# Optimization experiments

Measured on AMD Instinct MI355X. Metric: run time of the kernel, lower is better.

## Reference

```python
import jax, jax.numpy as jnp
import numpy as np

B, T, E, H, FF = 8, 1024, 1024, 16, 4096
HD = E // H
SCALE = HD ** -0.5
EPS = 1e-12  # LayerNorm eps from TransformerLayer


def layer_norm(x, w, b):
    u = x.mean(-1, keepdims=True)
    s = ((x - u) ** 2).mean(-1, keepdims=True)  # biased variance, as in module
    return w * (x - u) / jnp.sqrt(s + EPS) + b


def setup_inputs() -> dict:
    key = jax.random.key(0)
    ks = jax.random.split(key, 8)
    std = 0.02  # nn.init.normal_(std=0.02)
    x = jax.random.normal(ks[0], (B, T, E), jnp.float32)
    # padding mask: positions >= length are padding (1 = ignore); ensure no all-masked row
    lengths = jax.random.randint(ks[1], (B,), T // 2, T + 1)
    self_padding_mask = jnp.arange(T)[None, :] >= lengths[:, None]
    # causal mask from SelfAttentionMask: triu(ones, 1)
    attn_mask = jnp.triu(jnp.ones((T, T), dtype=bool), 1)
    in_w = std * jax.random.normal(ks[2], (3 * E, E), jnp.float32)
    in_b = jnp.zeros((3 * E,), jnp.float32)
    out_w = std * jax.random.normal(ks[3], (E, E), jnp.float32)
    out_b = jnp.zeros((E,), jnp.float32)
    fc1_w = std * jax.random.normal(ks[4], (FF, E), jnp.float32)
    fc1_b = jnp.zeros((FF,), jnp.float32)
    fc2_w = std * jax.random.normal(ks[5], (E, FF), jnp.float32)
    fc2_b = jnp.zeros((E,), jnp.float32)
    ln1_w = jnp.ones((E,), jnp.float32)
    ln1_b = jnp.zeros((E,), jnp.float32)
    ln2_w = jnp.ones((E,), jnp.float32)
    ln2_b = jnp.zeros((E,), jnp.float32)
    return dict(x=x, in_w=in_w, in_b=in_b, out_w=out_w, out_b=out_b,
                fc1_w=fc1_w, fc1_b=fc1_b, fc2_w=fc2_w, fc2_b=fc2_b,
                ln1_w=ln1_w, ln1_b=ln1_b, ln2_w=ln2_w, ln2_b=ln2_b,
                self_padding_mask=self_padding_mask, attn_mask=attn_mask)


def reference(x, in_w, in_b, out_w, out_b, fc1_w, fc1_b, fc2_w, fc2_b,
              ln1_w, ln1_b, ln2_w, ln2_b, self_padding_mask, attn_mask):
    b, t, e = x.shape
    # --- self attention sublayer ---
    residual = x
    qkv = x @ in_w.T + in_b                       # [B,T,3E] fused in_proj (qkv_same path)
    q, k, v = jnp.split(qkv, 3, axis=-1)
    q = (q * SCALE).reshape(b, t, H, HD)
    k = k.reshape(b, t, H, HD)
    v = v.reshape(b, t, H, HD)
    scores = jnp.einsum('bqhd,bkhd->bhqk', q, k)  # [B,H,T,T]
    mask = attn_mask[None, None, :, :] | self_padding_mask[:, None, None, :]
    scores = jnp.where(mask, -jnp.inf, scores)
    p = jax.nn.softmax(scores, axis=-1)
    attn = jnp.einsum('bhqk,bkhd->bqhd', p, v).reshape(b, t, e)
    attn = attn @ out_w.T + out_b
    x = layer_norm(residual + attn, ln1_w, ln1_b)
    # --- feed-forward sublayer ---
    residual = x
    h = jax.nn.relu(x @ fc1_w.T + fc1_b)
    x = layer_norm(residual + (h @ fc2_w.T + fc2_b), ln2_w, ln2_b)
    return x
```

## Files before the change

kernel.cpp:

```cpp
#include <hip/hip_runtime.h>

typedef unsigned short u16;
typedef __attribute__((ext_vector_type(8))) short short8;
typedef __attribute__((ext_vector_type(4))) short short4v;
typedef __attribute__((ext_vector_type(4))) float f32x4;

#define DEV static __device__ __forceinline__

DEV float bf2f(u16 h) {
    union { unsigned int u; float f; } v; v.u = ((unsigned int)h) << 16; return v.f;
}
DEV u16 f2bf(float f) {
    union { float f; unsigned int u; } v; v.f = f;
    unsigned int r = (v.u + 0x7fff + ((v.u >> 16) & 1)) >> 16;
    return (u16)r;
}
DEV float ldx(const void* p, size_t i, int f32) {
    return f32 ? ((const float*)p)[i] : bf2f(((const u16*)p)[i]);
}

#define GLD16(g, l) __builtin_amdgcn_global_load_lds( \
    (const __attribute__((address_space(1))) void*)(g), \
    (__attribute__((address_space(3))) void*)(l), 16, 0, 0)

#define STAGE(P, pf32, eoff, dst8) do {                                        \
    if (!(pf32)) { GLD16(((const u16*)(P)) + (eoff), (dst8)); }                \
    else {                                                                     \
        const float* _p = ((const float*)(P)) + (eoff);                        \
        f32x4 _a = *(const f32x4*)_p, _b = *(const f32x4*)(_p + 4);            \
        short8 _s;                                                             \
        _s[0]=(short)f2bf(_a[0]); _s[1]=(short)f2bf(_a[1]);                    \
        _s[2]=(short)f2bf(_a[2]); _s[3]=(short)f2bf(_a[3]);                    \
        _s[4]=(short)f2bf(_b[0]); _s[5]=(short)f2bf(_b[1]);                    \
        _s[6]=(short)f2bf(_b[2]); _s[7]=(short)f2bf(_b[3]);                    \
        *(short8*)(dst8) = _s;                                                 \
    } } while (0)

__global__ __launch_bounds__(64) void probe_kernel(
    const void* __restrict__ x, const void* __restrict__ pad,
    int* __restrict__ flags, int* __restrict__ flagsA)
{
    const int lane = threadIdx.x;
    const u16* xu = (const u16*)x;
    const unsigned int e = (xu[lane * 2] >> 7) & 0xFF;
    const int sane = (e >= 0x70 && e <= 0x8F) ? 1 : 0;
    unsigned long long m = __ballot(sane);
    const int f32 = (__popcll(m) < 32) ? 1 : 0;

    const unsigned int* pi = (const unsigned int*)pad;
    int bytes = 0;
#pragma unroll
    for (int j = 0; j < 6; j++) {
        unsigned int v = pi[128 + j * 64 + lane];
        if (v > 1u) bytes = 1;
    }
    m = __ballot(bytes);
    if (lane == 0) {
        flags[0] = f32; flags[1] = (m != 0ULL) ? 1 : 0;
        flagsA[0] = 0;  flagsA[1] = 0;
    }
}

__global__ __launch_bounds__(256) void conv4(
    const void* __restrict__ src, u16* __restrict__ dst, int n4,
    const int* __restrict__ flags)
{
    const int i = blockIdx.x * 256 + threadIdx.x;
    if (i >= n4) return;
    if (flags[0]) {
        f32x4 v = ((const f32x4*)src)[i];
        short4v s;
        s[0] = (short)f2bf(v[0]); s[1] = (short)f2bf(v[1]);
        s[2] = (short)f2bf(v[2]); s[3] = (short)f2bf(v[3]);
        ((short4v*)dst)[i] = s;
    } else {
        ((short4v*)dst)[i] = ((const short4v*)src)[i];
    }
}

__global__ __launch_bounds__(256) void mask_to_bias(
    const void* __restrict__ pad, float* __restrict__ out,
    const int* __restrict__ flags)
{
    const int i = blockIdx.x * 256 + threadIdx.x;
    const int mv = flags[1] ? (int)((const unsigned char*)pad)[i]
                            : ((const int*)pad)[i];
    out[i] = mv ? -1e30f : 0.0f;
}

#define GEMM_CORE(Av, ASEL, a_row0, Wv, w_off, ldw, K)                        \
    __shared__ __align__(16) u16 As[128 * 32];                                \
    __shared__ __align__(16) u16 Bs[128 * 32];                                \
    const int inf32 = flags[0];                                               \
    const int af32  = (ASEL) ? inf32 : 0;                                     \
    const int tid  = threadIdx.x;                                             \
    const int lane = tid & 63;                                                \
    const int wave = tid >> 6;                                                \
    const int lc   = lane & 15;                                               \
    const int quad = lane >> 4;                                               \
    const int m0 = blockIdx.x * 128;                                          \
    const int n0 = blockIdx.y * 128;                                          \
    const int wm = (wave >> 1) * 64;                                          \
    const int wn = (wave & 1) * 64;                                           \
    const int r0 = tid >> 2;                                                  \
    const int ko = (tid & 3) * 8;                                             \
    f32x4 acc[4][4] = {};                                                     \
    for (int k0 = 0; k0 < (K); k0 += 32) {                                    \
        STAGE(Av, af32, ((size_t)(a_row0) + m0 + r0) * (K) + k0 + ko,         \
              &As[tid * 8]);                                                  \
        STAGE(Av, af32, ((size_t)(a_row0) + m0 + r0 + 64) * (K) + k0 + ko,    \
              &As[2048 + tid * 8]);                                           \
        STAGE(Wv, inf32, (size_t)(w_off) + (size_t)(n0 + r0) * (ldw) + k0 + ko,\
              &Bs[tid * 8]);                                                  \
        STAGE(Wv, inf32, (size_t)(w_off) + (size_t)(n0 + r0 + 64) * (ldw) + k0 + ko,\
              &Bs[2048 + tid * 8]);                                           \
        __syncthreads();                                                      \
        short8 afr[4], bfr[4];                                                \
        const int qd = quad * 8;                                              \
        _Pragma("unroll")                                                     \
        for (int mt = 0; mt < 4; mt++)                                        \
            afr[mt] = *(const short8*)&As[(wm + mt * 16 + lc) * 32 + qd];     \
        _Pragma("unroll")                                                     \
        for (int nt = 0; nt < 4; nt++)                                        \
            bfr[nt] = *(const short8*)&Bs[(wn + nt * 16 + lc) * 32 + qd];     \
        _Pragma("unroll")                                                     \
        for (int mt = 0; mt < 4; mt++)                                        \
            _Pragma("unroll")                                                 \
            for (int nt = 0; nt < 4; nt++)                                    \
                acc[mt][nt] = __builtin_amdgcn_mfma_f32_16x16x32_bf16(        \
                    afr[mt], bfr[nt], acc[mt][nt], 0, 0, 0);                  \
        __syncthreads();                                                      \
    }                                                                         \
    const int ce0 = n0 + wn + lc;                                             \
    const int re0 = m0 + wm + quad * 4;

template<int EPI>
__global__ __launch_bounds__(256, 2) void gemm_bt(
    const void* __restrict__ A, int a_sel, long a_row0,
    const void* __restrict__ W, long w_off,
    const void* __restrict__ bias, long b_off,
    const void* __restrict__ resid, int r_sel, long r_row0,
    u16* __restrict__ C, long c_row0,
    int N, int K, int ldw, const int* __restrict__ flags)
{
    GEMM_CORE(A, a_sel, a_row0, W, w_off, ldw, K)
    const int rf32 = r_sel ? inf32 : 0;
#pragma unroll
    for (int mt = 0; mt < 4; mt++) {
#pragma unroll
        for (int nt = 0; nt < 4; nt++) {
            const int c = ce0 + nt * 16;
            const float bv = ldx(bias, (size_t)b_off + c, inf32);
#pragma unroll
            for (int i = 0; i < 4; i++) {
                const int r = re0 + mt * 16 + i;
                float v = acc[mt][nt][i] + bv;
                if (EPI == 1)
                    v += ldx(resid, ((size_t)r_row0 + r) * N + c, rf32);
                if (EPI == 2) v = fmaxf(v, 0.0f);
                C[((size_t)c_row0 + r) * N + c] = f2bf(v);
            }
        }
    }
}

__global__ __launch_bounds__(256, 2) void gemm_qkv(
    const void* __restrict__ A, long a_row0,
    const void* __restrict__ W, const void* __restrict__ bias,
    u16* __restrict__ Qo, u16* __restrict__ Ko, u16* __restrict__ Vt,
    const int* __restrict__ flags)
{
    GEMM_CORE(A, 1, a_row0, W, 0, 1024, 1024)
    if (n0 < 1024) {
#pragma unroll
        for (int mt = 0; mt < 4; mt++)
#pragma unroll
            for (int nt = 0; nt < 4; nt++) {
                const int c = ce0 + nt * 16;
                const float bv = ldx(bias, c, inf32);
#pragma unroll
                for (int i = 0; i < 4; i++) {
                    const int r = re0 + mt * 16 + i;
                    Qo[((size_t)a_row0 + r) * 1024 + c] =
                        f2bf((acc[mt][nt][i] + bv) * 0.125f);
                }
            }
    } else if (n0 < 2048) {
#pragma unroll
        for (int mt = 0; mt < 4; mt++)
#pragma unroll
            for (int nt = 0; nt < 4; nt++) {
                const int c = ce0 + nt * 16;
                const float bv = ldx(bias, c, inf32);
#pragma unroll
                for (int i = 0; i < 4; i++) {
                    const int r = re0 + mt * 16 + i;
                    Ko[(size_t)r * 1024 + (c - 1024)] = f2bf(acc[mt][nt][i] + bv);
                }
            }
    } else {
#pragma unroll
        for (int mt = 0; mt < 4; mt++)
#pragma unroll
            for (int nt = 0; nt < 4; nt++) {
                const int c = ce0 + nt * 16;
                const float bv = ldx(bias, c, inf32);
                const int cv = c - 2048;
                const int hh = cv >> 6, d = cv & 63;
                const int rb = re0 + mt * 16;
                const int bl = rb >> 10, t = rb & 1023;
                short4v pk;
#pragma unroll
                for (int i = 0; i < 4; i++)
                    pk[i] = (short)f2bf(acc[mt][nt][i] + bv);
                *(short4v*)&Vt[((size_t)(bl * 16 + hh) * 64 + d) * 1024 + t] = pk;
            }
    }
}

__global__ __launch_bounds__(256, 2) void gemm_accf32(
    const void* __restrict__ A, const void* __restrict__ W, long w_off,
    const void* __restrict__ bias, const u16* __restrict__ resid, long r_row0,
    float* __restrict__ C, int ldw, int init, const int* __restrict__ flags)
{
    GEMM_CORE(A, 0, 0, W, w_off, ldw, 1024)
#pragma unroll
    for (int mt = 0; mt < 4; mt++) {
#pragma unroll
        for (int nt = 0; nt < 4; nt++) {
            const int c = ce0 + nt * 16;
            const float bv = ldx(bias, c, inf32);
#pragma unroll
            for (int i = 0; i < 4; i++) {
                const int r = re0 + mt * 16 + i;
                float v = acc[mt][nt][i];
                if (init) v += bv + bf2f(resid[((size_t)r_row0 + r) * 1024 + c]);
                else      v += C[(size_t)r * 1024 + c];
                C[(size_t)r * 1024 + c] = v;
            }
        }
    }
}

#define GEMM8_PRE(Ag_, Wg_, Kg_)                                              \
    __shared__ __align__(16) u16 Ab[3][128 * 64];                             \
    __shared__ __align__(16) u16 Bb[3][256 * 64];                             \
    const u16* Ag = (Ag_); const u16* Wg = (Wg_); const int Kg = (Kg_);       \
    const int tid  = threadIdx.x;                                             \
    const int lane = tid & 63;                                                \
    const int lc   = lane & 15;                                               \
    const int quad = lane >> 4;                                               \
    const int w    = tid >> 6;                                                \
    const int wr   = w >> 2;                                                  \
    const int wc   = w & 3;                                                   \
    const int m0 = blockIdx.x * 128;                                          \
    const int n0 = blockIdx.y * 256;                                          \
    const int srow = tid >> 3;                                                \
    const int scol = (((tid & 7) ^ (srow & 7)) << 3);                         \
    const int sw0 = (((quad) ^ (lc & 7)) << 3);                               \
    const int sw1 = sw0 ^ 32;                                                 \
    f32x4 acc[4][4] = {};                                                     \
    short8 af[4], bf[4];

#define SA8(buf, kk) do {                                                     \
    GLD16(Ag + (size_t)(m0 + srow) * Kg + (kk) + scol, &Ab[buf][tid * 8]);    \
    GLD16(Ag + (size_t)(m0 + 64 + srow) * Kg + (kk) + scol,                   \
          &Ab[buf][4096 + tid * 8]); } while (0)
#define SB8a(buf, kk) do {                                                    \
    GLD16(Wg + (size_t)(n0 + srow) * Kg + (kk) + scol, &Bb[buf][tid * 8]);    \
    GLD16(Wg + (size_t)(n0 + 64 + srow) * Kg + (kk) + scol,                   \
          &Bb[buf][4096 + tid * 8]); } while (0)
#define SB8b(buf, kk) do {                                                    \
    GLD16(Wg + (size_t)(n0 + 128 + srow) * Kg + (kk) + scol,                  \
          &Bb[buf][8192 + tid * 8]);                                          \
    GLD16(Wg + (size_t)(n0 + 192 + srow) * Kg + (kk) + scol,                  \
          &Bb[buf][12288 + tid * 8]); } while (0)
#define LDFR(rbuf, SW) do { _Pragma("unroll")                                 \
    for (int q_ = 0; q_ < 4; q_++) {                                          \
        af[q_] = *(const short8*)&Ab[rbuf][(wr * 64 + q_ * 16 + lc) * 64 + (SW)];\
        bf[q_] = *(const short8*)&Bb[rbuf][(wc * 64 + q_ * 16 + lc) * 64 + (SW)];\
    } } while (0)
#define MFMA16 do { _Pragma("unroll")                                         \
    for (int mq = 0; mq < 4; mq++) { _Pragma("unroll")                        \
    for (int nq = 0; nq < 4; nq++)                                            \
        acc[mq][nq] = __builtin_amdgcn_mfma_f32_16x16x32_bf16(                \
            af[mq], bf[nq], acc[mq][nq], 0, 0, 0); } } while (0)

#define GEMM8_LOOP                                                            \
    const int NT = Kg >> 6;                                                   \
    SA8(0, 0); SB8a(0, 0); SB8b(0, 0);                                        \
    if (NT > 1) { SA8(1, 64); SB8a(1, 64); SB8b(1, 64); }                     \
    if (NT > 1) asm volatile("s_waitcnt vmcnt(6)" ::: "memory");              \
    else        asm volatile("s_waitcnt vmcnt(0)" ::: "memory");              \
    __builtin_amdgcn_s_barrier();                                             \
    int rb_ = 0, wb_ = 2;                                                     \
    for (int t = 0; t < NT; ++t) {                                            \
        const bool s_ = (t + 2 < NT);                                         \
        const int k2_ = (t + 2) << 6;                                         \
        LDFR(rb_, sw0);                                                       \
        if (s_) { SA8(wb_, k2_); SB8a(wb_, k2_); }                            \
        __builtin_amdgcn_s_barrier();                                         \
        asm volatile("s_waitcnt lgkmcnt(0)" ::: "memory");                    \
        __builtin_amdgcn_s_setprio(1);                                        \
        MFMA16;                                                               \
        __builtin_amdgcn_s_setprio(0);                                        \
        __builtin_amdgcn_s_barrier();                                         \
        LDFR(rb_, sw1);                                                       \
        if (s_) SB8b(wb_, k2_);                                               \
        __builtin_amdgcn_s_barrier();                                         \
        asm volatile("s_waitcnt lgkmcnt(0)" ::: "memory");                    \
        __builtin_amdgcn_s_setprio(1);                                        \
        MFMA16;                                                               \
        __builtin_amdgcn_s_setprio(0);                                        \
        if (s_) asm volatile("s_waitcnt vmcnt(6)" ::: "memory");              \
        else    asm volatile("s_waitcnt vmcnt(0)" ::: "memory");              \
        __builtin_amdgcn_s_barrier();                                         \
        rb_ = (rb_ == 2) ? 0 : rb_ + 1;                                      \
        wb_ = (wb_ == 2) ? 0 : wb_ + 1;                                      \
    }                                                                         \
    const int cb0 = n0 + wc * 64 + lc;                                        \
    const int rb0 = m0 + wr * 64 + quad * 4;

template<int EPI>
__global__ __launch_bounds__(512, 2) void gemm8(
    const u16* __restrict__ A, const u16* __restrict__ W,
    const u16* __restrict__ bias, const u16* __restrict__ resid,
    u16* __restrict__ C, int N, int K)
{
    GEMM8_PRE(A, W, K)
    GEMM8_LOOP
#pragma unroll
    for (int mq = 0; mq < 4; mq++) {
#pragma unroll
        for (int nq = 0; nq < 4; nq++) {
            const int cN = cb0 + nq * 16;
            const float bv = bf2f(bias[cN]);
#pragma unroll
            for (int i = 0; i < 4; i++) {
                const int rM = rb0 + mq * 16 + i;
                float v = acc[mq][nq][i] + bv;
                if (EPI == 1) v += bf2f(resid[(size_t)rM * N + cN]);
                if (EPI == 2) v = fmaxf(v, 0.0f);
                C[(size_t)rM * N + cN] = f2bf(v);
            }
        }
    }
}

#define GEMM256_PRE(Ag_, Wg_, Kg_)                                            \
    __shared__ __align__(16) u16 Ab[3][8192];                                 \
    __shared__ __align__(16) u16 Bb[3][8192];                                 \
    const u16* Ag = (Ag_); const u16* Wg = (Wg_); const int Kg = (Kg_);       \
    const int tid  = threadIdx.x;                                             \
    const int lane = tid & 63;                                                \
    const int lc   = lane & 15;                                               \
    const int quad = lane >> 4;                                               \
    const int w    = tid >> 6;                                                \
    const int wr   = w >> 2;                                                  \
    const int wc   = w & 3;                                                   \
    const int m0 = blockIdx.x * 256;                                          \
    const int n0 = blockIdx.y * 256;                                          \
    const int s_r = tid >> 2;                                                 \
    const int s_c = (((tid & 3) ^ ((tid >> 3) & 3)) << 3);                    \
    const int fsw = ((quad ^ ((lc >> 1) & 3)) << 3);                          \
    const int arow = wr * 128 + lc;                                           \
    const int brow = wc * 64 + lc;                                            \
    f32x4 acc[8][4] = {};                                                     \
    short8 af[4], bf[4];

#define SA256(buf, kk) do {                                                   \
    GLD16(Ag + (size_t)(m0 + s_r) * Kg + (kk) + s_c, &Ab[buf][tid * 8]);      \
    GLD16(Ag + (size_t)(m0 + 128 + s_r) * Kg + (kk) + s_c,                    \
          &Ab[buf][4096 + tid * 8]); } while (0)
#define SB256(buf, kk) do {                                                   \
    GLD16(Wg + (size_t)(n0 + s_r) * Kg + (kk) + s_c, &Bb[buf][tid * 8]);      \
    GLD16(Wg + (size_t)(n0 + 128 + s_r) * Kg + (kk) + s_c,                    \
          &Bb[buf][4096 + tid * 8]); } while (0)
#define LDA256(MH) do { _Pragma("unroll")                                     \
    for (int q_ = 0; q_ < 4; q_++)                                            \
        af[q_] = *(const short8*)                                             \
            &Ab[rb_][(arow + ((MH) * 4 + q_) * 16) * 32 + fsw]; } while (0)
#define LDB256 do { _Pragma("unroll")                                         \
    for (int q_ = 0; q_ < 4; q_++)                                            \
        bf[q_] = *(const short8*)                                             \
            &Bb[rb_][(brow + q_ * 16) * 32 + fsw]; } while (0)
#define MF256(MH) do { _Pragma("unroll")                                      \
    for (int mq = 0; mq < 4; mq++) { _Pragma("unroll")                        \
    for (int nq = 0; nq < 4; nq++)                                            \
        acc[(MH) * 4 + mq][nq] = __builtin_amdgcn_mfma_f32_16x16x32_bf16(     \
            af[mq], bf[nq], acc[(MH) * 4 + mq][nq], 0, 0, 0); } } while (0)

#define GEMM256_LOOP                                                          \
    const int NT = Kg >> 5;                                                   \
    SA256(0, 0); SB256(0, 0);                                                 \
    if (NT > 1) { SA256(1, 32); SB256(1, 32); }                               \
    if (NT > 1) asm volatile("s_waitcnt vmcnt(4)" ::: "memory");              \
    else        asm volatile("s_waitcnt vmcnt(0)" ::: "memory");              \
    __builtin_amdgcn_s_barrier();                                             \
    int rb_ = 0, wb_ = 2;                                                     \
    for (int t = 0; t < NT; ++t) {                                            \
        const bool s_ = (t + 2 < NT);                                         \
        const int k2_ = (t + 2) << 5;                                         \
        LDB256; LDA256(0);                                                    \
        if (s_) SA256(wb_, k2_);                                              \
        __builtin_amdgcn_s_barrier();                                         \
        asm volatile("s_waitcnt lgkmcnt(0)" ::: "memory");                    \
        __builtin_amdgcn_s_setprio(1);                                        \
        MF256(0);                                                             \
        __builtin_amdgcn_s_setprio(0);                                        \
        __builtin_amdgcn_s_barrier();                                         \
        LDA256(1);                                                            \
        if (s_) SB256(wb_, k2_);                                              \
        __builtin_amdgcn_s_barrier();                                         \
        asm volatile("s_waitcnt lgkmcnt(0)" ::: "memory");                    \
        __builtin_amdgcn_s_setprio(1);                                        \
        MF256(1);                                                             \
        __builtin_amdgcn_s_setprio(0);                                        \
        if (s_) asm volatile("s_waitcnt vmcnt(4)" ::: "memory");              \
        else    asm volatile("s_waitcnt vmcnt(0)" ::: "memory");              \
        __builtin_amdgcn_s_barrier();                                         \
        rb_ = (rb_ == 2) ? 0 : rb_ + 1;                                      \
        wb_ = (wb_ == 2) ? 0 : wb_ + 1;                                      \
    }                                                                         \
    const int cb0 = n0 + wc * 64 + lc;                                        \
    const int rb0 = m0 + wr * 128 + quad * 4;

template<int EPI>
__global__ __launch_bounds__(512, 2) void gemm256(
    const u16* __restrict__ A, const u16* __restrict__ W,
    const u16* __restrict__ bias, const u16* __restrict__ resid,
    u16* __restrict__ C, int N, int K)
{
    GEMM256_PRE(A, W, K)
    GEMM256_LOOP
#pragma unroll
    for (int mq = 0; mq < 8; mq++) {
#pragma unroll
        for (int nq = 0; nq < 4; nq++) {
            const int cN = cb0 + nq * 16;
            const float bv = bf2f(bias[cN]);
#pragma unroll
            for (int i = 0; i < 4; i++) {
                const int rM = rb0 + mq * 16 + i;
                float v = acc[mq][nq][i] + bv;
                if (EPI == 1) v += bf2f(resid[(size_t)rM * N + cN]);
                if (EPI == 2) v = fmaxf(v, 0.0f);
                C[(size_t)rM * N + cN] = f2bf(v);
            }
        }
    }
}

__global__ __launch_bounds__(512, 2) void gemm256_qkv(
    const u16* __restrict__ A, const u16* __restrict__ W,
    const u16* __restrict__ bias,
    u16* __restrict__ Qo, u16* __restrict__ Ko, u16* __restrict__ Vt)
{
    GEMM256_PRE(A, W, 1024)
    GEMM256_LOOP
    if (n0 < 1024) {
#pragma unroll
        for (int mq = 0; mq < 8; mq++)
#pragma unroll
            for (int nq = 0; nq < 4; nq++) {
                const int c = cb0 + nq * 16;
                const float bv = bf2f(bias[c]);
#pragma unroll
                for (int i = 0; i < 4; i++) {
                    const int r = rb0 + mq * 16 + i;
                    Qo[(size_t)r * 1024 + c] =
                        f2bf((acc[mq][nq][i] + bv) * 0.125f);
                }
            }
    } else if (n0 < 2048) {
#pragma unroll
        for (int mq = 0; mq < 8; mq++)
#pragma unroll
            for (int nq = 0; nq < 4; nq++) {
                const int c = cb0 + nq * 16;
                const float bv = bf2f(bias[c]);
#pragma unroll
                for (int i = 0; i < 4; i++) {
                    const int r = rb0 + mq * 16 + i;
                    Ko[(size_t)r * 1024 + (c - 1024)] =
                        f2bf(acc[mq][nq][i] + bv);
                }
            }
    } else {
#pragma unroll
        for (int mq = 0; mq < 8; mq++)
#pragma unroll
            for (int nq = 0; nq < 4; nq++) {
                const int c = cb0 + nq * 16;
                const float bv = bf2f(bias[c]);
                const int cv = c - 2048;
                const int hh = cv >> 6, d = cv & 63;
                const int rbase = rb0 + mq * 16;
                const int bl = rbase >> 10, tt = rbase & 1023;
                short4v pk;
#pragma unroll
                for (int i = 0; i < 4; i++)
                    pk[i] = (short)f2bf(acc[mq][nq][i] + bv);
                *(short4v*)&Vt[((size_t)(bl * 16 + hh) * 64 + d) * 1024 + tt] = pk;
            }
    }
}

__global__ __launch_bounds__(256, 2) void attn_kernel(
    u16* __restrict__ QO, const u16* __restrict__ Ko,
    const u16* __restrict__ Vt, const float* __restrict__ kb, int b0)
{
    __shared__ __align__(16) u16 Qs[2 * 128 * 32];
    __shared__ __align__(16) u16 Ks[2][2 * 64 * 32];
    __shared__ __align__(16) u16 Vs[2][2 * 64 * 32];
    __shared__ __align__(16) u16 Ps[4][32 * 72];
    __shared__ float kba[1024];

    const int tid  = threadIdx.x;
    const int lane = tid & 63;
    const int w    = tid >> 6;
    const int lc   = lane & 15;
    const int quad = lane >> 4;
    const int bl = blockIdx.y >> 4;
    const int h  = blockIdx.y & 15;
    const int b  = b0 + bl;

    *(f32x4*)&kba[tid * 4] = *(const f32x4*)&kb[b * 1024 + tid * 4];

    for (int p = 0; p < 2; p++) {
        const int qt = p ? 7 - (int)blockIdx.x : (int)blockIdx.x;

#pragma unroll
        for (int it = 0; it < 4; it++) {
            const int kcd = it >> 1, half = it & 1;
            const int r = half * 64 + (tid >> 2);
            const int c = kcd * 32 + (tid & 3) * 8;
            GLD16(&QO[((size_t)(b * 1024 + qt * 128 + r)) * 1024 + h * 64 + c],
                  &Qs[kcd * 4096 + half * 2048 + tid * 8]);
        }
        {
            const int rr = tid >> 2;
#pragma unroll
            for (int it = 0; it < 2; it++) {
                const int cc = it * 32 + (tid & 3) * 8;
                GLD16(&Ko[((size_t)(bl * 1024 + rr)) * 1024 + h * 64 + cc],
                      &Ks[0][it * 2048 + tid * 8]);
                GLD16(&Vt[((size_t)(bl * 16 + h) * 64 + rr) * 1024 + cc],
                      &Vs[0][it * 2048 + tid * 8]);
            }
        }
        __syncthreads();

        short8 aq[2][2];
#pragma unroll
        for (int mt = 0; mt < 2; mt++)
#pragma unroll
            for (int kc = 0; kc < 2; kc++)
                aq[mt][kc] = *(const short8*)
                    &Qs[kc * 4096 + (w * 32 + mt * 16 + lc) * 32 + quad * 8];

        f32x4 o[2][4] = {};
        float m_i[2][4], l_i[2][4];
#pragma unroll
        for (int mt = 0; mt < 2; mt++)
#pragma unroll
            for (int i = 0; i < 4; i++) { m_i[mt][i] = -1e30f; l_i[mt][i] = 0.0f; }

        const int ktmax = 2 * qt + 2;
        for (int kt = 0; kt < ktmax; kt++) {
            const int cur = kt & 1;
            if (kt + 1 < ktmax) {
                const int nxt = cur ^ 1;
                const int rr = tid >> 2;
#pragma unroll
                for (int it = 0; it < 2; it++) {
                    const int cc = it * 32 + (tid & 3) * 8;
                    GLD16(&Ko[((size_t)(bl * 1024 + (kt + 1) * 64 + rr)) * 1024 + h * 64 + cc],
                          &Ks[nxt][it * 2048 + tid * 8]);
                    GLD16(&Vt[((size_t)(bl * 16 + h) * 64 + rr) * 1024 + (kt + 1) * 64 + cc],
                          &Vs[nxt][it * 2048 + tid * 8]);
                }
            }

            short8 bk[4][2];
#pragma unroll
            for (int nt = 0; nt < 4; nt++)
#pragma unroll
                for (int kc = 0; kc < 2; kc++)
                    bk[nt][kc] = *(const short8*)
                        &Ks[cur][kc * 2048 + (nt * 16 + lc) * 32 + quad * 8];

            f32x4 s[2][4];
#pragma unroll
            for (int mt = 0; mt < 2; mt++)
#pragma unroll
                for (int nt = 0; nt < 4; nt++) {
                    f32x4 z = {};
#pragma unroll
                    for (int kc = 0; kc < 2; kc++)
                        z = __builtin_amdgcn_mfma_f32_16x16x32_bf16(
                            aq[mt][kc], bk[nt][kc], z, 0, 0, 0);
                    s[mt][nt] = z;
                }

            const int causal = (kt >= 2 * qt);
            float al[2][4];
#pragma unroll
            for (int mt = 0; mt < 2; mt++) {
                const int qg0 = qt * 128 + w * 32 + mt * 16 + quad * 4;
#pragma unroll
                for (int nt = 0; nt < 4; nt++) {
                    const int kg = kt * 64 + nt * 16 + lc;
                    const float kbv = kba[kt * 64 + nt * 16 + lc];
#pragma unroll
                    for (int i = 0; i < 4; i++) {
                        float sv = s[mt][nt][i] + kbv;
                        if (causal && kg > qg0 + i) sv = -1e30f;
                        s[mt][nt][i] = sv;
                    }
                }
                float mnew[4], rs[4];
#pragma unroll
                for (int i = 0; i < 4; i++) {
                    float rm = fmaxf(fmaxf(s[mt][0][i], s[mt][1][i]),
                                     fmaxf(s[mt][2][i], s[mt][3][i]));
                    rm = fmaxf(rm, __shfl_xor(rm, 1));
                    rm = fmaxf(rm, __shfl_xor(rm, 2));
                    rm = fmaxf(rm, __shfl_xor(rm, 4));
                    rm = fmaxf(rm, __shfl_xor(rm, 8));
                    mnew[i] = fmaxf(m_i[mt][i], rm);
                    al[mt][i] = exp2f((m_i[mt][i] - mnew[i]) * 1.442695041f);
                    rs[i] = 0.0f;
                }
#pragma unroll
                for (int nt = 0; nt < 4; nt++)
#pragma unroll
                    for (int i = 0; i < 4; i++) {
                        float pp = exp2f((s[mt][nt][i] - mnew[i]) * 1.442695041f);
                        s[mt][nt][i] = pp;
                        rs[i] += pp;
                    }
#pragma unroll
                for (int i = 0; i < 4; i++) {
                    float r = rs[i];
                    r += __shfl_xor(r, 1);
                    r += __shfl_xor(r, 2);
                    r += __shfl_xor(r, 4);
                    r += __shfl_xor(r, 8);
                    l_i[mt][i] = l_i[mt][i] * al[mt][i] + r;
                    m_i[mt][i] = mnew[i];
                }
#pragma unroll
                for (int nt = 0; nt < 4; nt++)
#pragma unroll
                    for (int i = 0; i < 4; i++)
                        Ps[w][(mt * 16 + quad * 4 + i) * 72 + nt * 16 + lc] =
                            f2bf(s[mt][nt][i]);
            }

            short8 ap[2][2], bv2[4][2];
#pragma unroll
            for (int mt = 0; mt < 2; mt++)
#pragma unroll
                for (int kc = 0; kc < 2; kc++)
                    ap[mt][kc] = *(const short8*)
                        &Ps[w][(mt * 16 + lc) * 72 + kc * 32 + quad * 8];
#pragma unroll
            for (int nt = 0; nt < 4; nt++)
#pragma unroll
                for (int kc = 0; kc < 2; kc++)
                    bv2[nt][kc] = *(const short8*)
                        &Vs[cur][kc * 2048 + (nt * 16 + lc) * 32 + quad * 8];
#pragma unroll
            for (int mt = 0; mt < 2; mt++)
#pragma unroll
                for (int nt = 0; nt < 4; nt++) {
                    f32x4 oo = o[mt][nt];
#pragma unroll
                    for (int i = 0; i < 4; i++) oo[i] *= al[mt][i];
#pragma unroll
                    for (int kc = 0; kc < 2; kc++)
                        oo = __builtin_amdgcn_mfma_f32_16x16x32_bf16(
                            ap[mt][kc], bv2[nt][kc], oo, 0, 0, 0);
                    o[mt][nt] = oo;
                }
            __syncthreads();
        }

#pragma unroll
        for (int mt = 0; mt < 2; mt++)
#pragma unroll
            for (int i = 0; i < 4; i++) {
                const float inv = l_i[mt][i] > 0.0f ? 1.0f / l_i[mt][i] : 0.0f;
#pragma unroll
                for (int nt = 0; nt < 4; nt++) {
                    const int r = qt * 128 + w * 32 + mt * 16 + quad * 4 + i;
                    const int d = nt * 16 + lc;
                    QO[((size_t)(b * 1024 + r)) * 1024 + h * 64 + d] =
                        f2bf(o[mt][nt][i] * inv);
                }
            }
    }
}

template<int IN16, int OUTSEL>
__global__ __launch_bounds__(256) void ln_kernel(
    const void* __restrict__ yv, const void* __restrict__ w,
    const void* __restrict__ bb, void* __restrict__ o, long o_row0,
    const int* __restrict__ flags)
{
    const int row = blockIdx.x;
    const int tid = threadIdx.x;
    const int inf32 = flags[0];
    float x0, x1, x2, x3;
    if (IN16) {
        const u16* p = (const u16*)yv + (size_t)row * 1024 + tid * 4;
        short4v v = *(const short4v*)p;
        x0 = bf2f((u16)v[0]); x1 = bf2f((u16)v[1]);
        x2 = bf2f((u16)v[2]); x3 = bf2f((u16)v[3]);
    } else {
        const float* p = (const float*)yv + (size_t)row * 1024 + tid * 4;
        f32x4 v = *(const f32x4*)p;
        x0 = v[0]; x1 = v[1]; x2 = v[2]; x3 = v[3];
    }
    float s = x0 + x1 + x2 + x3;
    float q = x0 * x0 + x1 * x1 + x2 * x2 + x3 * x3;
#pragma unroll
    for (int off = 32; off; off >>= 1) {
        s += __shfl_xor(s, off);
        q += __shfl_xor(q, off);
    }
    __shared__ float sm[8];
    const int lane = tid & 63, wv = tid >> 6;
    if (lane == 0) { sm[wv] = s; sm[4 + wv] = q; }
    __syncthreads();
    const float ts = sm[0] + sm[1] + sm[2] + sm[3];
    const float tq = sm[4] + sm[5] + sm[6] + sm[7];
    const float mean = ts * (1.0f / 1024.0f);
    float var = tq * (1.0f / 1024.0f) - mean * mean;
    if (var < 0.0f) var = 0.0f;
    const float rinv = rsqrtf(var + 1e-12f);

    const size_t obase = ((size_t)o_row0 + row) * 1024 + tid * 4;
#pragma unroll
    for (int j = 0; j < 4; j++) {
        const int c = tid * 4 + j;
        float xv = (j == 0) ? x0 : (j == 1) ? x1 : (j == 2) ? x2 : x3;
        float v = ldx(w, c, inf32) * ((xv - mean) * rinv) + ldx(bb, c, inf32);
        if (OUTSEL && inf32) ((float*)o)[obase + j] = v;
        else                 ((u16*)o)[obase + j] = f2bf(v);
    }
}

extern "C" void kernel_launch(void* const* d_in, const int* in_sizes, int n_in,
                              void* d_out, int out_size, void* d_ws, size_t ws_size,
                              hipStream_t stream)
{
    const void* x     = d_in[0];
    const void* in_w  = d_in[1];
    const void* in_b  = d_in[2];
    const void* out_w = d_in[3];
    const void* out_b = d_in[4];
    const void* fc1_w = d_in[5];
    const void* fc1_b = d_in[6];
    const void* fc2_w = d_in[7];
    const void* fc2_b = d_in[8];
    const void* ln1w  = d_in[9];
    const void* ln1b  = d_in[10];
    const void* ln2w  = d_in[11];
    const void* ln2b  = d_in[12];
    const void* pad   = d_in[13];
    u16* outp = (u16*)d_out;
    char* ws = (char*)d_ws;
    dim3 blk(256);
    dim3 blk8(512);

    const size_t MB = 1024 * 1024;
    const bool bigWS = ws_size >= (105 * MB + 64 * 1024);

    if (bigWS) {
        u16*   xb   = (u16*)(ws + 0);
        u16*   x1   = (u16*)(ws + 0);
        u16*   w1b  = (u16*)(ws + 16 * MB);
        u16*   wob  = (u16*)(ws + 22 * MB);
        u16*   f1b  = (u16*)(ws + 24 * MB);
        u16*   f2b  = (u16*)(ws + 32 * MB);
        u16*   inbb = (u16*)(ws + 40 * MB);
        u16*   outbb= (u16*)(ws + 40 * MB + 8192);
        u16*   f1bb = (u16*)(ws + 40 * MB + 16384);
        u16*   f2bb = (u16*)(ws + 40 * MB + 24576);
        u16*   Ko   = (u16*)(ws + 41 * MB);
        u16*   Vt   = (u16*)(ws + 57 * MB);
        u16*   y1   = (u16*)(ws + 73 * MB);
        u16*   h    = (u16*)(ws + 41 * MB);
        u16*   y2   = (u16*)(ws + 16 * MB);
        int*   flags  = (int*)(ws + 105 * MB);
        int*   flagsA = (int*)(ws + 105 * MB + 32);
        float* kbias  = (float*)(ws + 105 * MB + 64);

        probe_kernel<<<dim3(1), dim3(64), 0, stream>>>(x, pad, flags, flagsA);
        mask_to_bias<<<dim3(32), blk, 0, stream>>>(pad, kbias, flags);
        conv4<<<dim3(8192), blk, 0, stream>>>(x, xb, 2097152, flags);
        conv4<<<dim3(3072), blk, 0, stream>>>(in_w, w1b, 786432, flags);
        conv4<<<dim3(1024), blk, 0, stream>>>(out_w, wob, 262144, flags);
        conv4<<<dim3(4096), blk, 0, stream>>>(fc1_w, f1b, 1048576, flags);
        conv4<<<dim3(4096), blk, 0, stream>>>(fc2_w, f2b, 1048576, flags);
        conv4<<<dim3(3), blk, 0, stream>>>(in_b, inbb, 768, flags);
        conv4<<<dim3(1), blk, 0, stream>>>(out_b, outbb, 256, flags);
        conv4<<<dim3(4), blk, 0, stream>>>(fc1_b, f1bb, 1024, flags);
        conv4<<<dim3(1), blk, 0, stream>>>(fc2_b, f2bb, 256, flags);

        gemm256_qkv<<<dim3(32, 12), blk8, 0, stream>>>(
            xb, w1b, inbb, outp, Ko, Vt);
        attn_kernel<<<dim3(4, 128), blk, 0, stream>>>(outp, Ko, Vt, kbias, 0);
        gemm8<1><<<dim3(64, 4), blk8, 0, stream>>>(
            outp, wob, outbb, xb, y1, 1024, 1024);
        ln_kernel<1, 0><<<dim3(8192), blk, 0, stream>>>(y1, ln1w, ln1b, x1, 0, flags);
        gemm256<2><<<dim3(32, 16), blk8, 0, stream>>>(
            x1, f1b, f1bb, nullptr, h, 4096, 1024);
        gemm8<1><<<dim3(64, 4), blk8, 0, stream>>>(
            h, f2b, f2bb, x1, y2, 1024, 4096);
        ln_kernel<1, 1><<<dim3(8192), blk, 0, stream>>>(y2, ln2w, ln2b, d_out, 0, flags);
    } else {
        u16*   Ko    = (u16*)(ws + 0);
        u16*   Vt    = (u16*)(ws + 4 * MB);
        u16*   y1h   = (u16*)(ws + 0);
        float* acc   = (float*)(ws + 0);
        u16*   hc    = (u16*)(ws + 8 * MB);
        int*   flags  = (int*)(ws + 12 * MB);
        int*   flagsA = (int*)(ws + 12 * MB + 32);
        float* kbias  = (float*)(ws + 12 * MB + 64);

        probe_kernel<<<dim3(1), dim3(64), 0, stream>>>(x, pad, flags, flagsA);
        mask_to_bias<<<dim3(32), blk, 0, stream>>>(pad, kbias, flags);

        for (int q = 0; q < 4; q++) {
            const long r0 = (long)q * 2048;
            gemm_qkv<<<dim3(16, 24), blk, 0, stream>>>(
                x, r0, in_w, in_b, outp, Ko, Vt, flags);
            attn_kernel<<<dim3(4, 32), blk, 0, stream>>>(
                outp, Ko, Vt, kbias, q * 2);
        }
        for (int hf = 0; hf < 2; hf++) {
            const long r0 = (long)hf * 4096;
            gemm_bt<1><<<dim3(32, 8), blk, 0, stream>>>(
                outp, 0, r0, out_w, 0, out_b, 0, x, 1, r0,
                y1h, 0, 1024, 1024, 1024, flags);
            ln_kernel<1, 0><<<dim3(4096), blk, 0, stream>>>(
                y1h, ln1w, ln1b, outp, r0, flags);
        }
        for (int q = 3; q >= 0; q--) {
            const long r0 = (long)q * 2048;
            for (int c = 0; c < 4; c++) {
                gemm_bt<2><<<dim3(16, 8), blk, 0, stream>>>(
                    outp, 0, r0, fc1_w, (long)c * 1024 * 1024, fc1_b, (long)c * 1024,
                    nullptr, 0, 0, hc, 0, 1024, 1024, 1024, flags);
                gemm_accf32<<<dim3(16, 8), blk, 0, stream>>>(
                    hc, fc2_w, (long)c * 1024, fc2_b, outp, r0,
                    acc, 4096, c == 0, flags);
            }
            ln_kernel<0, 1><<<dim3(2048), blk, 0, stream>>>(
                acc, ln2w, ln2b, d_out, r0, flags);
        }
    }
}
```

Before: 524.2 us.

## Streamline attention softmax with log2-folded scale and MFMA row sums

Folds log2(e) into the Q scaling in both QKV GEMM epilogues, so the softmax can call exp2 directly without a multiply per element. The row sums of P are now computed by an MFMA against a ones vector instead of shuffle reductions; the sums are then read from lane 0 of each group at the end. It also packs the bf16 conversion of P with v_cvt_pk_bf16, applies the causal mask only on diagonal tiles, and skips rescaling the output accumulator when no row max changed in the wave. Together these cut VALU and cross-lane work in the attention inner loop. The cost is an extra MFMA per tile and row sums taken from the bf16-rounded P.

```diff
diff --git a/kernel.cpp b/kernel.cpp
--- a/kernel.cpp
+++ b/kernel.cpp
@@ -18,6 +18,8 @@
 DEV float ldx(const void* p, size_t i, int f32) {
     return f32 ? ((const float*)p)[i] : bf2f(((const u16*)p)[i]);
 }
+
+#define QSCL 0.18033688011112042f
 
 #define GLD16(g, l) __builtin_amdgcn_global_load_lds( \
     (const __attribute__((address_space(1))) void*)(g), \
@@ -182,7 +184,7 @@
                 for (int i = 0; i < 4; i++) {
                     const int r = re0 + mt * 16 + i;
                     Qo[((size_t)a_row0 + r) * 1024 + c] =
-                        f2bf((acc[mt][nt][i] + bv) * 0.125f);
+                        f2bf((acc[mt][nt][i] + bv) * QSCL);
                 }
             }
     } else if (n0 < 2048) {
@@ -469,7 +471,7 @@
                 for (int i = 0; i < 4; i++) {
                     const int r = rb0 + mq * 16 + i;
                     Qo[(size_t)r * 1024 + c] =
-                        f2bf((acc[mq][nq][i] + bv) * 0.125f);
+                        f2bf((acc[mq][nq][i] + bv) * QSCL);
                 }
             }
     } else if (n0 < 2048) {
@@ -524,6 +526,13 @@
     const int bl = blockIdx.y >> 4;
     const int h  = blockIdx.y & 15;
     const int b  = b0 + bl;
+
+    short8 bsum;
+    {
+        const short ov = (lc == 0) ? (short)0x3F80 : (short)0;
+#pragma unroll
+        for (int j = 0; j < 8; j++) bsum[j] = ov;
+    }
 
     *(f32x4*)&kba[tid * 4] = *(const f32x4*)&kb[b * 1024 + tid * 4];
 
@@ -603,23 +612,32 @@
                     s[mt][nt] = z;
                 }
 
-            const int causal = (kt >= 2 * qt);
+#pragma unroll
+            for (int mt = 0; mt < 2; mt++)
+#pragma unroll
+                for (int nt = 0; nt < 4; nt++) {
+                    const float kbv = kba[kt * 64 + nt * 16 + lc];
+#pragma unroll
+                    for (int i = 0; i < 4; i++) s[mt][nt][i] += kbv;
+                }
+            if (kt >= 2 * qt) {
+#pragma unroll
+                for (int mt = 0; mt < 2; mt++) {
+                    const int qg0 = qt * 128 + w * 32 + mt * 16 + quad * 4;
+#pragma unroll
+                    for (int nt = 0; nt < 4; nt++) {
+                        const int kg = kt * 64 + nt * 16 + lc;
+#pragma unroll
+                        for (int i = 0; i < 4; i++)
+                            if (kg > qg0 + i) s[mt][nt][i] = -1e30f;
+                    }
+                }
+            }
+
             float al[2][4];
 #pragma unroll
             for (int mt = 0; mt < 2; mt++) {
-                const int qg0 = qt * 128 + w * 32 + mt * 16 + quad * 4;
-#pragma unroll
-                for (int nt = 0; nt < 4; nt++) {
-                    const int kg = kt * 64 + nt * 16 + lc;
-                    const float kbv = kba[kt * 64 + nt * 16 + lc];
-#pragma unroll
-                    for (int i = 0; i < 4; i++) {
-                        float sv = s[mt][nt][i] + kbv;
-                        if (causal && kg > qg0 + i) sv = -1e30f;
-                        s[mt][nt][i] = sv;
-                    }
-                }
-                float mnew[4], rs[4];
+                float mnew[4];
 #pragma unroll
                 for (int i = 0; i < 4; i++) {
                     float rm = fmaxf(fmaxf(s[mt][0][i], s[mt][1][i]),
@@ -628,35 +646,38 @@
                     rm = fmaxf(rm, __shfl_xor(rm, 2));
                     rm = fmaxf(rm, __shfl_xor(rm, 4));
                     rm = fmaxf(rm, __shfl_xor(rm, 8));
-                    mnew[i] = fmaxf(m_i[mt][i], rm);
-                    al[mt][i] = exp2f((m_i[mt][i] - mnew[i]) * 1.442695041f);
-                    rs[i] = 0.0f;
+                    const float mn = fmaxf(m_i[mt][i], rm);
+                    al[mt][i] = exp2f(m_i[mt][i] - mn);
+                    m_i[mt][i] = mn;
+                    mnew[i] = mn;
                 }
 #pragma unroll
                 for (int nt = 0; nt < 4; nt++)
 #pragma unroll
-                    for (int i = 0; i < 4; i++) {
-                        float pp = exp2f((s[mt][nt][i] - mnew[i]) * 1.442695041f);
-                        s[mt][nt][i] = pp;
-                        rs[i] += pp;
+                    for (int i = 0; i < 4; i++)
+                        s[mt][nt][i] = exp2f(s[mt][nt][i] - mnew[i]);
+#pragma unroll
+                for (int nt = 0; nt < 4; nt++) {
+#pragma unroll
+                    for (int i2 = 0; i2 < 2; i2++) {
+                        unsigned int pk;
+                        asm("v_cvt_pk_bf16_f32 %0, %1, %2"
+                            : "=v"(pk)
+                            : "v"(s[mt][nt][2 * i2]), "v"(s[mt][nt][2 * i2 + 1]));
+                        Ps[w][(mt * 16 + quad * 4 + 2 * i2) * 72 + nt * 16 + lc] =
+                            (u16)pk;
+                        Ps[w][(mt * 16 + quad * 4 + 2 * i2 + 1) * 72 + nt * 16 + lc] =
+                            (u16)(pk >> 16);
                     }
-#pragma unroll
-                for (int i = 0; i < 4; i++) {
-                    float r = rs[i];
-                    r += __shfl_xor(r, 1);
-                    r += __shfl_xor(r, 2);
-                    r += __shfl_xor(r, 4);
-                    r += __shfl_xor(r, 8);
-                    l_i[mt][i] = l_i[mt][i] * al[mt][i] + r;
-                    m_i[mt][i] = mnew[i];
-                }
-#pragma unroll
-                for (int nt = 0; nt < 4; nt++)
-#pragma unroll
-                    for (int i = 0; i < 4; i++)
-                        Ps[w][(mt * 16 + quad * 4 + i) * 72 + nt * 16 + lc] =
-                            f2bf(s[mt][nt][i]);
-            }
+                }
+            }
+            int chg = 0;
+#pragma unroll
+            for (int mt = 0; mt < 2; mt++)
+#pragma unroll
+                for (int i = 0; i < 4; i++)
+                    chg |= (al[mt][i] != 1.0f) ? 1 : 0;
+            const int dor = __any(chg);
 
             short8 ap[2][2], bv2[4][2];
 #pragma unroll
@@ -671,19 +692,36 @@
                 for (int kc = 0; kc < 2; kc++)
                     bv2[nt][kc] = *(const short8*)
                         &Vs[cur][kc * 2048 + (nt * 16 + lc) * 32 + quad * 8];
+
+            f32x4 ls[2] = {};
+#pragma unroll
+            for (int mt = 0; mt < 2; mt++)
+#pragma unroll
+                for (int kc = 0; kc < 2; kc++)
+                    ls[mt] = __builtin_amdgcn_mfma_f32_16x16x32_bf16(
+                        ap[mt][kc], bsum, ls[mt], 0, 0, 0);
+
 #pragma unroll
             for (int mt = 0; mt < 2; mt++)
 #pragma unroll
                 for (int nt = 0; nt < 4; nt++) {
                     f32x4 oo = o[mt][nt];
-#pragma unroll
-                    for (int i = 0; i < 4; i++) oo[i] *= al[mt][i];
+                    if (dor) {
+#pragma unroll
+                        for (int i = 0; i < 4; i++) oo[i] *= al[mt][i];
+                    }
 #pragma unroll
                     for (int kc = 0; kc < 2; kc++)
                         oo = __builtin_amdgcn_mfma_f32_16x16x32_bf16(
                             ap[mt][kc], bv2[nt][kc], oo, 0, 0, 0);
                     o[mt][nt] = oo;
                 }
+#pragma unroll
+            for (int mt = 0; mt < 2; mt++)
+#pragma unroll
+                for (int i = 0; i < 4; i++)
+                    l_i[mt][i] = l_i[mt][i] * al[mt][i] + ls[mt][i];
+
             __syncthreads();
         }
 
@@ -691,7 +729,8 @@
         for (int mt = 0; mt < 2; mt++)
 #pragma unroll
             for (int i = 0; i < 4; i++) {
-                const float inv = l_i[mt][i] > 0.0f ? 1.0f / l_i[mt][i] : 0.0f;
+                const float lv = __shfl(l_i[mt][i], (lane & 48));
+                const float inv = lv > 0.0f ? 1.0f / lv : 0.0f;
 #pragma unroll
                 for (int nt = 0; nt < 4; nt++) {
                     const int r = qt * 128 + w * 32 + mt * 16 + quad * 4 + i;
```

Result: no change. 517.4 us (-1.3%).
